# Optimization experiments

Measured on AMD Instinct MI355X. Metric: run time of the kernel, lower is better.

## Reference

```python
import jax, jax.numpy as jnp
import numpy as np

NUM_CLASSES = 100000
EMBED_DIM = 512
BATCH = 16384
ALPHA = 0.95  # center update momentum: diff = (1 - ALPHA) * (centers - features)


def setup_inputs() -> dict:
    key = jax.random.key(0)
    k1, k2, k3 = jax.random.split(key, 3)
    features = jax.random.normal(k1, (BATCH, EMBED_DIM), dtype=jnp.float32)
    labels = jax.random.randint(k2, (BATCH,), 0, NUM_CLASSES, dtype=jnp.int64)
    center_var = jax.random.normal(k3, (NUM_CLASSES, EMBED_DIM), dtype=jnp.float32)
    return {"features": features, "labels": labels, "center_var": center_var}


def reference(features, labels, center_var):
    # gather per-label centers: [B, D]
    labels = labels.reshape(-1)
    centers_batch = center_var[labels]
    # update delta, 0.05 * (center - feature)
    diff = (1.0 - ALPHA) * (centers_batch - features)
    # scatter-subtract with duplicate-label accumulation (tf scatter_nd_sub semantics)
    new_centers = center_var.at[labels].add(-diff)
    # MSE between features and their (pre-update) centers
    loss = jnp.mean(jnp.square(features - centers_batch))
    return loss, new_centers
```

## Files before the change

kernel.cpp:

```cpp
#include <hip/hip_runtime.h>

constexpr int NUM_CLASSES  = 100000;
constexpr int EMBED_DIM    = 512;
constexpr int BATCH        = 16384;
constexpr int CENTER_ELEMS = NUM_CLASSES * EMBED_DIM;
constexpr int NSLOTS       = 256;
constexpr float UPDATE_SCALE = 0.05f;
constexpr float INV_COUNT  = 1.0f / 8388608.0f;


constexpr size_t WS_NEEDED = (size_t)NUM_CLASSES * 8 + NSLOTS * 4;

__global__ void zero_ws_kernel(int* __restrict__ counts, float* __restrict__ partials) {
    int g = blockIdx.x * blockDim.x + threadIdx.x;
    if (g < NUM_CLASSES) counts[g] = 0;
    if (g < NSLOTS) partials[g] = 0.0f;
}

__global__ void hist_kernel(const int* __restrict__ labels,
                            int* __restrict__ counts,
                            int* __restrict__ itemof) {
    int b = blockIdx.x * blockDim.x + threadIdx.x;
    if (b < BATCH) {
        int l = labels[b];
        atomicAdd(&counts[l], 1);
        itemof[l] = b;
    }
}

__global__ __launch_bounds__(128) void fused_rows_kernel(
        const float* __restrict__ features,
        const float* __restrict__ centers,
        const int*   __restrict__ counts,
        const int*   __restrict__ itemof,
        float* __restrict__ out,
        float* __restrict__ partials) {
    const int c = blockIdx.x;
    const int t = threadIdx.x;
    const int cnt = counts[c];

    const float4 c4 = ((const float4*)(centers + (size_t)c * EMBED_DIM))[t];
    float4 n4 = c4;

    __shared__ float row[EMBED_DIM];

    if (cnt == 1) {
        const int b = itemof[c];
        const float4 f4 = ((const float4*)(features + (size_t)b * EMBED_DIM))[t];
        float4 d;
        d.x = f4.x - c4.x;
        d.y = f4.y - c4.y;
        d.z = f4.z - c4.z;
        d.w = f4.w - c4.w;
        n4.x = fmaf(UPDATE_SCALE, d.x, c4.x);
        n4.y = fmaf(UPDATE_SCALE, d.y, c4.y);
        n4.z = fmaf(UPDATE_SCALE, d.z, c4.z);
        n4.w = fmaf(UPDATE_SCALE, d.w, c4.w);
        float local = d.x * d.x + d.y * d.y + d.z * d.z + d.w * d.w;
        #pragma unroll
        for (int off = 32; off > 0; off >>= 1)
            local += __shfl_down(local, off, 64);
        if ((t & 63) == 0)
            atomicAdd(&partials[(c * 2 + (t >> 6)) & (NSLOTS - 1)], local);
    }

    ((float4*)row)[t] = n4;
    __syncthreads();

    const size_t R = (size_t)c * EMBED_DIM;
    if (t < 127) {
        float4 o;
        o.x = row[4 * t + 3];
        o.y = row[4 * t + 4];
        o.z = row[4 * t + 5];
        o.w = row[4 * t + 6];
        ((float4*)(out + R + 4))[t] = o;
    } else {
        out[R + 1] = row[0];
        out[R + 2] = row[1];
        out[R + 3] = row[2];
        out[R + EMBED_DIM] = row[EMBED_DIM - 1];
    }
}

__global__ __launch_bounds__(128) void dup_update_kernel(
        const float* __restrict__ features,
        const int*   __restrict__ labels,
        const float* __restrict__ centers,
        const int*   __restrict__ counts,
        float* __restrict__ out,
        float* __restrict__ partials) {
    const int b = blockIdx.x;
    const int l = labels[b];
    if (counts[l] < 2) return;
    const int t = threadIdx.x;

    const float4 f4 = ((const float4*)(features + (size_t)b * EMBED_DIM))[t];
    const float4 c4 = ((const float4*)(centers + (size_t)l * EMBED_DIM))[t];
    float4 d;
    d.x = f4.x - c4.x;
    d.y = f4.y - c4.y;
    d.z = f4.z - c4.z;
    d.w = f4.w - c4.w;

    float* nrow = out + 1 + (size_t)l * EMBED_DIM + (size_t)t * 4;
    atomicAdd(nrow + 0, UPDATE_SCALE * d.x);
    atomicAdd(nrow + 1, UPDATE_SCALE * d.y);
    atomicAdd(nrow + 2, UPDATE_SCALE * d.z);
    atomicAdd(nrow + 3, UPDATE_SCALE * d.w);

    float local = d.x * d.x + d.y * d.y + d.z * d.z + d.w * d.w;
    #pragma unroll
    for (int off = 32; off > 0; off >>= 1)
        local += __shfl_down(local, off, 64);
    if ((t & 63) == 0)
        atomicAdd(&partials[(b * 2 + (t >> 6)) & (NSLOTS - 1)], local);
}

__global__ __launch_bounds__(64) void finalize_loss_kernel(
        const float* __restrict__ partials,
        float* __restrict__ out) {
    float v = 0.0f;
    #pragma unroll
    for (int k = 0; k < NSLOTS / 64; ++k)
        v += partials[threadIdx.x + k * 64];
    #pragma unroll
    for (int off = 32; off > 0; off >>= 1)
        v += __shfl_down(v, off, 64);
    if (threadIdx.x == 0)
        out[0] = v * INV_COUNT;
}


__global__ void copy_centers_kernel(const float* __restrict__ src,
                                    float* __restrict__ dst,
                                    float* __restrict__ ws_partials) {
    int gid = blockIdx.x * blockDim.x + threadIdx.x;
    if (gid < NSLOTS) ws_partials[gid] = 0.0f;
    int stride = gridDim.x * blockDim.x;
    for (int i = gid; i < CENTER_ELEMS; i += stride) dst[i] = src[i];
}

__global__ __launch_bounds__(128) void update_kernel(
        const float* __restrict__ features,
        const int*   __restrict__ labels,
        const float* __restrict__ centers,
        float* __restrict__ out,
        float* __restrict__ ws_partials) {
    const int b = blockIdx.x;
    const int label = labels[b];
    const int t = threadIdx.x;
    const float4 f = ((const float4*)(features + (size_t)b * EMBED_DIM))[t];
    const float4 c = ((const float4*)(centers + (size_t)label * EMBED_DIM))[t];
    float4 d;
    d.x = f.x - c.x; d.y = f.y - c.y; d.z = f.z - c.z; d.w = f.w - c.w;
    float* nrow = out + 1 + (size_t)label * EMBED_DIM + (size_t)t * 4;
    atomicAdd(nrow + 0, UPDATE_SCALE * d.x);
    atomicAdd(nrow + 1, UPDATE_SCALE * d.y);
    atomicAdd(nrow + 2, UPDATE_SCALE * d.z);
    atomicAdd(nrow + 3, UPDATE_SCALE * d.w);
    float local = d.x * d.x + d.y * d.y + d.z * d.z + d.w * d.w;
    #pragma unroll
    for (int off = 32; off > 0; off >>= 1)
        local += __shfl_down(local, off, 64);
    if ((t & 63) == 0)
        atomicAdd(&ws_partials[(b * 2 + (t >> 6)) & (NSLOTS - 1)], local);
}


extern "C" void kernel_launch(void* const* d_in, const int* in_sizes, int n_in,
                              void* d_out, int out_size, void* d_ws, size_t ws_size,
                              hipStream_t stream) {
    const float* features = (const float*)d_in[0];
    const int*   labels   = (const int*)d_in[1];
    const float* centers  = (const float*)d_in[2];
    float* out = (float*)d_out;

    if (ws_size >= WS_NEEDED) {
        int*   counts   = (int*)d_ws;
        int*   itemof   = counts + NUM_CLASSES;
        float* partials = (float*)(itemof + NUM_CLASSES);

        zero_ws_kernel<<<(NUM_CLASSES + 255) / 256, 256, 0, stream>>>(counts, partials);
        hist_kernel<<<(BATCH + 255) / 256, 256, 0, stream>>>(labels, counts, itemof);
        fused_rows_kernel<<<NUM_CLASSES, 128, 0, stream>>>(features, centers, counts,
                                                           itemof, out, partials);
        dup_update_kernel<<<BATCH, 128, 0, stream>>>(features, labels, centers,
                                                     counts, out, partials);
        finalize_loss_kernel<<<1, 64, 0, stream>>>(partials, out);
    } else {
        float* partials = (float*)d_ws;
        copy_centers_kernel<<<8192, 256, 0, stream>>>(centers, out + 1, partials);
        update_kernel<<<BATCH, 128, 0, stream>>>(features, labels, centers, out, partials);
        finalize_loss_kernel<<<1, 64, 0, stream>>>(partials, out);
    }
}
```

Baseline: 389.7 us.

## Bucket up to eight items per class and fold duplicate updates into row pass

```diff
diff --git a/kernel.cpp b/kernel.cpp
--- a/kernel.cpp
+++ b/kernel.cpp
@@ -5,11 +5,17 @@
 constexpr int BATCH        = 16384;
 constexpr int CENTER_ELEMS = NUM_CLASSES * EMBED_DIM;
 constexpr int NSLOTS       = 256;
+constexpr int KMAX         = 8;
 constexpr float UPDATE_SCALE = 0.05f;
 constexpr float INV_COUNT  = 1.0f / 8388608.0f;
 
-
-constexpr size_t WS_NEEDED = (size_t)NUM_CLASSES * 8 + NSLOTS * 4;
+typedef float f4 __attribute__((ext_vector_type(4)));
+
+constexpr size_t WS_NEW = (size_t)NUM_CLASSES * 4
+                        + (size_t)NUM_CLASSES * KMAX * 4
+                        + (size_t)NSLOTS * 4;
+
+constexpr size_t WS_OLD = (size_t)NUM_CLASSES * 8 + NSLOTS * 4;
 
 __global__ void zero_ws_kernel(int* __restrict__ counts, float* __restrict__ partials) {
     int g = blockIdx.x * blockDim.x + threadIdx.x;
@@ -19,7 +25,119 @@
 
 __global__ void hist_kernel(const int* __restrict__ labels,
                             int* __restrict__ counts,
-                            int* __restrict__ itemof) {
+                            int* __restrict__ items) {
+    int b = blockIdx.x * blockDim.x + threadIdx.x;
+    if (b < BATCH) {
+        int l = labels[b];
+        int r = atomicAdd(&counts[l], 1);
+        if (r < KMAX) items[l * KMAX + r] = b;
+    }
+}
+
+__global__ __launch_bounds__(256) void fused_rows_kernel(
+        const float* __restrict__ features,
+        const float* __restrict__ centers,
+        const int*   __restrict__ counts,
+        const int*   __restrict__ items,
+        float* __restrict__ out,
+        float* __restrict__ partials) {
+    const int t    = threadIdx.x;
+    const int half = t >> 7;
+    const int ts   = t & 127;
+    const int c    = blockIdx.x * 2 + half;
+    const int cnt  = counts[c];
+
+    const f4 c4 = __builtin_nontemporal_load(
+        (const f4*)(centers + (size_t)c * EMBED_DIM) + ts);
+    f4 n4 = c4;
+
+    if (cnt > 0 && cnt <= KMAX) {
+        f4 s; s.x = 0.f; s.y = 0.f; s.z = 0.f; s.w = 0.f;
+        float local = 0.0f;
+        for (int i = 0; i < cnt; ++i) {
+            const int b = items[c * KMAX + i];
+            const f4 f = __builtin_nontemporal_load(
+                (const f4*)(features + (size_t)b * EMBED_DIM) + ts);
+            float dx = f.x - c4.x;
+            float dy = f.y - c4.y;
+            float dz = f.z - c4.z;
+            float dw = f.w - c4.w;
+            s.x += dx; s.y += dy; s.z += dz; s.w += dw;
+            local += dx * dx + dy * dy + dz * dz + dw * dw;
+        }
+        n4.x = fmaf(UPDATE_SCALE, s.x, c4.x);
+        n4.y = fmaf(UPDATE_SCALE, s.y, c4.y);
+        n4.z = fmaf(UPDATE_SCALE, s.z, c4.z);
+        n4.w = fmaf(UPDATE_SCALE, s.w, c4.w);
+        #pragma unroll
+        for (int off = 32; off > 0; off >>= 1)
+            local += __shfl_down(local, off, 64);
+        if ((t & 63) == 0)
+            atomicAdd(&partials[(c * 2 + (ts >> 6)) & (NSLOTS - 1)], local);
+    }
+
+    __shared__ float row[2 * EMBED_DIM];
+    ((f4*)row)[t] = n4;
+    __syncthreads();
+
+    const size_t R0 = (size_t)blockIdx.x * (2 * EMBED_DIM);
+    if (t < 255) {
+        f4 o;
+        o.x = row[4 * t + 3];
+        o.y = row[4 * t + 4];
+        o.z = row[4 * t + 5];
+        o.w = row[4 * t + 6];
+        __builtin_nontemporal_store(o, (f4*)(out + R0 + 4) + t);
+    } else {
+        out[R0 + 1] = row[0];
+        out[R0 + 2] = row[1];
+        out[R0 + 3] = row[2];
+        out[R0 + 2 * EMBED_DIM] = row[2 * EMBED_DIM - 1];
+    }
+}
+
+__global__ __launch_bounds__(256) void overflow_kernel(
+        const float* __restrict__ features,
+        const int*   __restrict__ labels,
+        const float* __restrict__ centers,
+        const int*   __restrict__ counts,
+        float* __restrict__ out,
+        float* __restrict__ partials) {
+    const int b = blockIdx.x * blockDim.x + threadIdx.x;
+    if (b >= BATCH) return;
+    const int l = labels[b];
+    if (counts[l] <= KMAX) return;
+    const int seg = blockIdx.y;
+    const float* f  = features + (size_t)b * EMBED_DIM + seg * 64;
+    const float* cr = centers  + (size_t)l * EMBED_DIM + seg * 64;
+    float* nrow = out + 1 + (size_t)l * EMBED_DIM + seg * 64;
+    float local = 0.0f;
+    for (int j = 0; j < 64; ++j) {
+        float d = f[j] - cr[j];
+        local += d * d;
+        atomicAdd(nrow + j, UPDATE_SCALE * d);
+    }
+    atomicAdd(&partials[(b * 8 + seg) & (NSLOTS - 1)], local);
+}
+
+__global__ __launch_bounds__(64) void finalize_loss_kernel(
+        const float* __restrict__ partials,
+        float* __restrict__ out) {
+    float v = 0.0f;
+    #pragma unroll
+    for (int k = 0; k < NSLOTS / 64; ++k)
+        v += partials[threadIdx.x + k * 64];
+    #pragma unroll
+    for (int off = 32; off > 0; off >>= 1)
+        v += __shfl_down(v, off, 64);
+    if (threadIdx.x == 0)
+        out[0] = v * INV_COUNT;
+}
+
+
+__global__ void hist1_kernel(const int* __restrict__ labels,
+                             int* __restrict__ counts,
+                             int* __restrict__ itemof) {
     int b = blockIdx.x * blockDim.x + threadIdx.x;
     if (b < BATCH) {
         int l = labels[b];
@@ -28,7 +146,7 @@
     }
 }
 
-__global__ __launch_bounds__(128) void fused_rows_kernel(
+__global__ __launch_bounds__(128) void fused_rows1_kernel(
         const float* __restrict__ features,
         const float* __restrict__ centers,
         const int*   __restrict__ counts,
@@ -46,12 +164,12 @@
 
     if (cnt == 1) {
         const int b = itemof[c];
-        const float4 f4 = ((const float4*)(features + (size_t)b * EMBED_DIM))[t];
+        const float4 f4v = ((const float4*)(features + (size_t)b * EMBED_DIM))[t];
         float4 d;
-        d.x = f4.x - c4.x;
-        d.y = f4.y - c4.y;
-        d.z = f4.z - c4.z;
-        d.w = f4.w - c4.w;
+        d.x = f4v.x - c4.x;
+        d.y = f4v.y - c4.y;
+        d.z = f4v.z - c4.z;
+        d.w = f4v.w - c4.w;
         n4.x = fmaf(UPDATE_SCALE, d.x, c4.x);
         n4.y = fmaf(UPDATE_SCALE, d.y, c4.y);
         n4.z = fmaf(UPDATE_SCALE, d.z, c4.z);
@@ -95,13 +213,13 @@
     if (counts[l] < 2) return;
     const int t = threadIdx.x;
 
-    const float4 f4 = ((const float4*)(features + (size_t)b * EMBED_DIM))[t];
+    const float4 f4v = ((const float4*)(features + (size_t)b * EMBED_DIM))[t];
     const float4 c4 = ((const float4*)(centers + (size_t)l * EMBED_DIM))[t];
     float4 d;
-    d.x = f4.x - c4.x;
-    d.y = f4.y - c4.y;
-    d.z = f4.z - c4.z;
-    d.w = f4.w - c4.w;
+    d.x = f4v.x - c4.x;
+    d.y = f4v.y - c4.y;
+    d.z = f4v.z - c4.z;
+    d.w = f4v.w - c4.w;
 
     float* nrow = out + 1 + (size_t)l * EMBED_DIM + (size_t)t * 4;
     atomicAdd(nrow + 0, UPDATE_SCALE * d.x);
@@ -115,20 +233,6 @@
         local += __shfl_down(local, off, 64);
     if ((t & 63) == 0)
         atomicAdd(&partials[(b * 2 + (t >> 6)) & (NSLOTS - 1)], local);
-}
-
-__global__ __launch_bounds__(64) void finalize_loss_kernel(
-        const float* __restrict__ partials,
-        float* __restrict__ out) {
-    float v = 0.0f;
-    #pragma unroll
-    for (int k = 0; k < NSLOTS / 64; ++k)
-        v += partials[threadIdx.x + k * 64];
-    #pragma unroll
-    for (int off = 32; off > 0; off >>= 1)
-        v += __shfl_down(v, off, 64);
-    if (threadIdx.x == 0)
-        out[0] = v * INV_COUNT;
 }
 
 
@@ -176,15 +280,27 @@
     const float* centers  = (const float*)d_in[2];
     float* out = (float*)d_out;
 
-    if (ws_size >= WS_NEEDED) {
+    if (ws_size >= WS_NEW) {
+        int*   counts   = (int*)d_ws;
+        int*   items    = counts + NUM_CLASSES;
+        float* partials = (float*)(items + (size_t)NUM_CLASSES * KMAX);
+
+        zero_ws_kernel<<<(NUM_CLASSES + 255) / 256, 256, 0, stream>>>(counts, partials);
+        hist_kernel<<<(BATCH + 255) / 256, 256, 0, stream>>>(labels, counts, items);
+        fused_rows_kernel<<<NUM_CLASSES / 2, 256, 0, stream>>>(features, centers, counts,
+                                                               items, out, partials);
+        overflow_kernel<<<dim3(BATCH / 256, 8), 256, 0, stream>>>(features, labels, centers,
+                                                                  counts, out, partials);
+        finalize_loss_kernel<<<1, 64, 0, stream>>>(partials, out);
+    } else if (ws_size >= WS_OLD) {
         int*   counts   = (int*)d_ws;
         int*   itemof   = counts + NUM_CLASSES;
         float* partials = (float*)(itemof + NUM_CLASSES);
 
         zero_ws_kernel<<<(NUM_CLASSES + 255) / 256, 256, 0, stream>>>(counts, partials);
-        hist_kernel<<<(BATCH + 255) / 256, 256, 0, stream>>>(labels, counts, itemof);
-        fused_rows_kernel<<<NUM_CLASSES, 128, 0, stream>>>(features, centers, counts,
-                                                           itemof, out, partials);
+        hist1_kernel<<<(BATCH + 255) / 256, 256, 0, stream>>>(labels, counts, itemof);
+        fused_rows1_kernel<<<NUM_CLASSES, 128, 0, stream>>>(features, centers, counts,
+                                                            itemof, out, partials);
         dup_update_kernel<<<BATCH, 128, 0, stream>>>(features, labels, centers,
                                                      counts, out, partials);
         finalize_loss_kernel<<<1, 64, 0, stream>>>(partials, out);
```

After: 362.8 us. 1.07x faster.

## Split into bulk shifted copy plus per-touched-class update with bucketed items

Applied to the files above, without the earlier changes.

```diff
diff --git a/kernel.cpp b/kernel.cpp
--- a/kernel.cpp
+++ b/kernel.cpp
@@ -5,116 +5,139 @@
 constexpr int BATCH        = 16384;
 constexpr int CENTER_ELEMS = NUM_CLASSES * EMBED_DIM;
 constexpr int NSLOTS       = 256;
+constexpr int KMAX         = 8;
 constexpr float UPDATE_SCALE = 0.05f;
 constexpr float INV_COUNT  = 1.0f / 8388608.0f;
 
-
-constexpr size_t WS_NEEDED = (size_t)NUM_CLASSES * 8 + NSLOTS * 4;
-
-__global__ void zero_ws_kernel(int* __restrict__ counts, float* __restrict__ partials) {
+typedef float f4 __attribute__((ext_vector_type(4)));
+
+constexpr size_t WS_COUNTS_OFF  = 0;
+constexpr size_t WS_ITEMS_OFF   = WS_COUNTS_OFF + (size_t)NUM_CLASSES;
+constexpr size_t WS_TOUCHED_OFF = WS_ITEMS_OFF + (size_t)NUM_CLASSES * KMAX;
+constexpr size_t WS_NTOUCH_OFF  = WS_TOUCHED_OFF + (size_t)BATCH;
+constexpr size_t WS_PART_OFF    = WS_NTOUCH_OFF + 16;
+constexpr size_t WS_NEW         = (WS_PART_OFF + NSLOTS) * 4;
+
+__global__ void zero_ws_kernel(int* __restrict__ counts,
+                               int* __restrict__ ntouched,
+                               float* __restrict__ partials) {
     int g = blockIdx.x * blockDim.x + threadIdx.x;
     if (g < NUM_CLASSES) counts[g] = 0;
+    if (g == 0) *ntouched = 0;
     if (g < NSLOTS) partials[g] = 0.0f;
 }
 
 __global__ void hist_kernel(const int* __restrict__ labels,
                             int* __restrict__ counts,
-                            int* __restrict__ itemof) {
+                            int* __restrict__ items,
+                            int* __restrict__ touched,
+                            int* __restrict__ ntouched) {
     int b = blockIdx.x * blockDim.x + threadIdx.x;
     if (b < BATCH) {
         int l = labels[b];
-        atomicAdd(&counts[l], 1);
-        itemof[l] = b;
-    }
-}
-
-__global__ __launch_bounds__(128) void fused_rows_kernel(
+        int r = atomicAdd(&counts[l], 1);
+        if (r < KMAX) items[l * KMAX + r] = b;
+        if (r == 0) {
+            int s = atomicAdd(ntouched, 1);
+            touched[s] = l;
+        }
+    }
+}
+
+__global__ __launch_bounds__(256) void copy_shift_kernel(
+        const float* __restrict__ src,
+        float* __restrict__ out) {
+    constexpr int NF4 = CENTER_ELEMS / 4;
+    const int gid    = blockIdx.x * blockDim.x + threadIdx.x;
+    const int stride = gridDim.x * blockDim.x;
+    int j = gid;
+    if (gid == 0) {
+        out[1] = src[0];
+        out[2] = src[1];
+        out[3] = src[2];
+        out[CENTER_ELEMS] = src[CENTER_ELEMS - 1];
+        j = stride;
+    }
+    for (; j < NF4; j += stride) {
+        const float* p = src + 4 * j - 1;
+        f4 v;
+        v.x = p[0];
+        v.y = p[1];
+        v.z = p[2];
+        v.w = p[3];
+        __builtin_nontemporal_store(v, (f4*)out + j);
+    }
+}
+
+__global__ __launch_bounds__(128) void touched_update_kernel(
         const float* __restrict__ features,
+        const int*   __restrict__ labels,
         const float* __restrict__ centers,
         const int*   __restrict__ counts,
-        const int*   __restrict__ itemof,
+        const int*   __restrict__ items,
+        const int*   __restrict__ touched,
+        const int*   __restrict__ ntouched,
         float* __restrict__ out,
         float* __restrict__ partials) {
-    const int c = blockIdx.x;
-    const int t = threadIdx.x;
+    const int nb = *ntouched;
+    if (blockIdx.x >= nb) return;
+    const int c   = touched[blockIdx.x];
     const int cnt = counts[c];
-
-    const float4 c4 = ((const float4*)(centers + (size_t)c * EMBED_DIM))[t];
-    float4 n4 = c4;
+    const int t   = threadIdx.x;
+
+    const f4 c4 = ((const f4*)(centers + (size_t)c * EMBED_DIM))[t];
+    f4 s; s.x = 0.f; s.y = 0.f; s.z = 0.f; s.w = 0.f;
+    float local = 0.0f;
+
+    if (cnt <= KMAX) {
+        for (int i = 0; i < cnt; ++i) {
+            const int b = items[c * KMAX + i];
+            const f4 f = ((const f4*)(features + (size_t)b * EMBED_DIM))[t];
+            float dx = f.x - c4.x, dy = f.y - c4.y, dz = f.z - c4.z, dw = f.w - c4.w;
+            s.x += dx; s.y += dy; s.z += dz; s.w += dw;
+            local += dx * dx + dy * dy + dz * dz + dw * dw;
+        }
+    } else {
+        for (int b = 0; b < BATCH; ++b) {
+            if (labels[b] == c) {
+                const f4 f = ((const f4*)(features + (size_t)b * EMBED_DIM))[t];
+                float dx = f.x - c4.x, dy = f.y - c4.y, dz = f.z - c4.z, dw = f.w - c4.w;
+                s.x += dx; s.y += dy; s.z += dz; s.w += dw;
+                local += dx * dx + dy * dy + dz * dz + dw * dw;
+            }
+        }
+    }
+
+    f4 n4;
+    n4.x = fmaf(UPDATE_SCALE, s.x, c4.x);
+    n4.y = fmaf(UPDATE_SCALE, s.y, c4.y);
+    n4.z = fmaf(UPDATE_SCALE, s.z, c4.z);
+    n4.w = fmaf(UPDATE_SCALE, s.w, c4.w);
+
+    #pragma unroll
+    for (int off = 32; off > 0; off >>= 1)
+        local += __shfl_down(local, off, 64);
+    if ((t & 63) == 0)
+        atomicAdd(&partials[(blockIdx.x * 2 + (t >> 6)) & (NSLOTS - 1)], local);
 
     __shared__ float row[EMBED_DIM];
-
-    if (cnt == 1) {
-        const int b = itemof[c];
-        const float4 f4 = ((const float4*)(features + (size_t)b * EMBED_DIM))[t];
-        float4 d;
-        d.x = f4.x - c4.x;
-        d.y = f4.y - c4.y;
-        d.z = f4.z - c4.z;
-        d.w = f4.w - c4.w;
-        n4.x = fmaf(UPDATE_SCALE, d.x, c4.x);
-        n4.y = fmaf(UPDATE_SCALE, d.y, c4.y);
-        n4.z = fmaf(UPDATE_SCALE, d.z, c4.z);
-        n4.w = fmaf(UPDATE_SCALE, d.w, c4.w);
-        float local = d.x * d.x + d.y * d.y + d.z * d.z + d.w * d.w;
-        #pragma unroll
-        for (int off = 32; off > 0; off >>= 1)
-            local += __shfl_down(local, off, 64);
-        if ((t & 63) == 0)
-            atomicAdd(&partials[(c * 2 + (t >> 6)) & (NSLOTS - 1)], local);
-    }
-
-    ((float4*)row)[t] = n4;
+    ((f4*)row)[t] = n4;
     __syncthreads();
 
     const size_t R = (size_t)c * EMBED_DIM;
     if (t < 127) {
-        float4 o;
+        f4 o;
         o.x = row[4 * t + 3];
         o.y = row[4 * t + 4];
         o.z = row[4 * t + 5];
         o.w = row[4 * t + 6];
-        ((float4*)(out + R + 4))[t] = o;
+        ((f4*)(out + R + 4))[t] = o;
     } else {
         out[R + 1] = row[0];
         out[R + 2] = row[1];
         out[R + 3] = row[2];
         out[R + EMBED_DIM] = row[EMBED_DIM - 1];
     }
-}
-
-__global__ __launch_bounds__(128) void dup_update_kernel(
-        const float* __restrict__ features,
-        const int*   __restrict__ labels,
-        const float* __restrict__ centers,
-        const int*   __restrict__ counts,
-        float* __restrict__ out,
-        float* __restrict__ partials) {
-    const int b = blockIdx.x;
-    const int l = labels[b];
-    if (counts[l] < 2) return;
-    const int t = threadIdx.x;
-
-    const float4 f4 = ((const float4*)(features + (size_t)b * EMBED_DIM))[t];
-    const float4 c4 = ((const float4*)(centers + (size_t)l * EMBED_DIM))[t];
-    float4 d;
-    d.x = f4.x - c4.x;
-    d.y = f4.y - c4.y;
-    d.z = f4.z - c4.z;
-    d.w = f4.w - c4.w;
-
-    float* nrow = out + 1 + (size_t)l * EMBED_DIM + (size_t)t * 4;
-    atomicAdd(nrow + 0, UPDATE_SCALE * d.x);
-    atomicAdd(nrow + 1, UPDATE_SCALE * d.y);
-    atomicAdd(nrow + 2, UPDATE_SCALE * d.z);
-    atomicAdd(nrow + 3, UPDATE_SCALE * d.w);
-
-    float local = d.x * d.x + d.y * d.y + d.z * d.z + d.w * d.w;
-    #pragma unroll
-    for (int off = 32; off > 0; off >>= 1)
-        local += __shfl_down(local, off, 64);
-    if ((t & 63) == 0)
-        atomicAdd(&partials[(b * 2 + (t >> 6)) & (NSLOTS - 1)], local);
 }
 
 __global__ __launch_bounds__(64) void finalize_loss_kernel(
@@ -176,17 +199,22 @@
     const float* centers  = (const float*)d_in[2];
     float* out = (float*)d_out;
 
-    if (ws_size >= WS_NEEDED) {
-        int*   counts   = (int*)d_ws;
-        int*   itemof   = counts + NUM_CLASSES;
-        float* partials = (float*)(itemof + NUM_CLASSES);
-
-        zero_ws_kernel<<<(NUM_CLASSES + 255) / 256, 256, 0, stream>>>(counts, partials);
-        hist_kernel<<<(BATCH + 255) / 256, 256, 0, stream>>>(labels, counts, itemof);
-        fused_rows_kernel<<<NUM_CLASSES, 128, 0, stream>>>(features, centers, counts,
-                                                           itemof, out, partials);
-        dup_update_kernel<<<BATCH, 128, 0, stream>>>(features, labels, centers,
-                                                     counts, out, partials);
+    if (ws_size >= WS_NEW) {
+        int* wsi       = (int*)d_ws;
+        int* counts    = wsi + WS_COUNTS_OFF;
+        int* items     = wsi + WS_ITEMS_OFF;
+        int* touched   = wsi + WS_TOUCHED_OFF;
+        int* ntouched  = wsi + WS_NTOUCH_OFF;
+        float* partials = (float*)(wsi + WS_PART_OFF);
+
+        zero_ws_kernel<<<(NUM_CLASSES + 255) / 256, 256, 0, stream>>>(
+            counts, ntouched, partials);
+        hist_kernel<<<(BATCH + 255) / 256, 256, 0, stream>>>(
+            labels, counts, items, touched, ntouched);
+        copy_shift_kernel<<<2048, 256, 0, stream>>>(centers, out);
+        touched_update_kernel<<<BATCH, 128, 0, stream>>>(
+            features, labels, centers, counts, items, touched, ntouched,
+            out, partials);
         finalize_loss_kernel<<<1, 64, 0, stream>>>(partials, out);
     } else {
         float* partials = (float*)d_ws;
```

New measurement: 426.7 us. +9.5%, slower.
